# Optimization experiments

Measured on AMD Instinct MI355X. Metric: run time of the kernel, lower is better.

Reference implementation:

```python
import jax, jax.numpy as jnp
import numpy as np

# Standard minigrid color mapping (module references global COLOR_TO_IDX)
COLOR_TO_IDX = {'red': 0, 'green': 1, 'blue': 2, 'purple': 3, 'yellow': 4, 'grey': 5}
AGENT_FEATURE_SIZE = 13
NUM_AGENTS_PER_COLOR = {'grey': 4, 'yellow': 4}
COLOR_ORDER = sorted(NUM_AGENTS_PER_COLOR.keys())  # ['grey', 'yellow']
FEATURE_DIM = 256
B, N = 131072, 16
INPUT_DIM = (1 + sum(NUM_AGENTS_PER_COLOR.values())) * AGENT_FEATURE_SIZE  # 117


def setup_inputs() -> dict:
    key = jax.random.key(0)
    ks = jax.random.split(key, 14)
    inp = {
        'query_position': jax.random.normal(ks[0], (B, 2), jnp.float32),
        'query_direction': jax.random.normal(ks[1], (B, 4), jnp.float32),
        'query_abilities': jax.random.normal(ks[2], (B, 2), jnp.float32),
        'query_carried': jax.random.normal(ks[3], (B, 2), jnp.float32),
        'query_status': jax.random.normal(ks[4], (B, 3), jnp.float32),
        'all_agent_positions': jax.random.normal(ks[5], (B, N, 2), jnp.float32),
        'all_agent_directions': jax.random.normal(ks[6], (B, N, 4), jnp.float32),
        'all_agent_abilities': jax.random.normal(ks[7], (B, N, 2), jnp.float32),
        'all_agent_carried': jax.random.normal(ks[8], (B, N, 2), jnp.float32),
        'all_agent_status': jax.random.normal(ks[9], (B, N, 3), jnp.float32),
        'agent_color_indices': jax.random.randint(ks[10], (B, N), 0, 6, jnp.int32),
        # fc params; W stored (in, out) so y = x @ W + b (same math as torch Linear)
        'W': jax.random.normal(ks[11], (INPUT_DIM, FEATURE_DIM), jnp.float32) / np.sqrt(INPUT_DIM),
        'b': jax.random.normal(ks[12], (FEATURE_DIM,), jnp.float32) * 0.01,
    }
    return inp


def reference(query_position, query_direction, query_abilities, query_carried,
              query_status, all_agent_positions, all_agent_directions,
              all_agent_abilities, all_agent_carried, all_agent_status,
              agent_color_indices, W, b):
    batch = query_position.shape[0]
    # (B, N, 13) per-agent features, (B, 13) query features
    F = jnp.concatenate([all_agent_positions, all_agent_directions,
                         all_agent_abilities, all_agent_carried,
                         all_agent_status], axis=-1)
    query = jnp.concatenate([query_position, query_direction, query_abilities,
                             query_carried, query_status], axis=-1)
    feats = [query]
    rows = jnp.arange(batch)[:, None]  # (B, 1) for batched scatter
    for color in COLOR_ORDER:
        cidx = COLOR_TO_IDX[color]
        M = NUM_AGENTS_PER_COLOR[color]
        mask = agent_color_indices == cidx                 # (B, N)
        rank = jnp.cumsum(mask, axis=1) - 1                # slot of each matching agent
        valid = mask & (rank < M)
        slot = jnp.where(valid, rank, M)                   # dump overflow/non-match into slot M
        out = jnp.zeros((batch, M + 1, AGENT_FEATURE_SIZE), F.dtype)
        out = out.at[rows, slot].set(F)                    # unique (b, slot) per valid agent
        feats.append(out[:, :M].reshape(batch, M * AGENT_FEATURE_SIZE))
    x = jnp.concatenate(feats, axis=1)                     # (B, 117)
    return jax.nn.relu(x @ W + b)
```

## Files before the change

kernel.cpp:

```cpp
#include <hip/hip_runtime.h>


#define TM 128
#define XS_LD 136
#define THREADS 512
#define NCOL 256

typedef short short8 __attribute__((ext_vector_type(8)));
typedef float f32x4 __attribute__((ext_vector_type(4)));

__device__ __forceinline__ short f2bf(float x) {
    unsigned u = __builtin_bit_cast(unsigned, x);
    unsigned r = (u + 0x7fffu + ((u >> 16) & 1u)) >> 16;
    return (short)r;
}
__device__ __forceinline__ unsigned pk2(float a, float b) {
    return (unsigned)(unsigned short)f2bf(a) | ((unsigned)(unsigned short)f2bf(b) << 16);
}

__global__ __launch_bounds__(256)
void swz_w_kernel(const float* __restrict__ W, short* __restrict__ Wb) {
    const int idx  = blockIdx.x * 256 + threadIdx.x;
    const int j    = idx & 7;
    const int lane = (idx >> 3) & 63;
    const int ct   = (idx >> 9) & 3;
    const int kt   = (idx >> 11) & 3;
    const int cg   = (idx >> 13) & 3;
    const int kk   = kt * 32 + (lane >> 4) * 8 + j;
    const int u    = kk / 14;
    const int f    = kk - u * 14;
    const int col  = cg * 64 + ct * 16 + (lane & 15);
    float v = 0.f;
    if (u < 9 && f < 13) v = W[(u * 13 + f) * NCOL + col];
    Wb[idx] = f2bf(v);
}

template<bool WS>
__global__ __launch_bounds__(THREADS, 4)
void mga_encoder_kernel(const float* __restrict__ qpos, const float* __restrict__ qdir,
                        const float* __restrict__ qabil, const float* __restrict__ qcarr,
                        const float* __restrict__ qstat,
                        const float* __restrict__ apos, const float* __restrict__ adir,
                        const float* __restrict__ aabil, const float* __restrict__ acarr,
                        const float* __restrict__ astat,
                        const int* __restrict__ cidx,
                        const float* __restrict__ W, const float* __restrict__ bvec,
                        const short* __restrict__ Wb,
                        float* __restrict__ out) {
    __shared__ __align__(16) short Xs[TM * XS_LD];

    const int tid  = threadIdx.x;
    const int wave = tid >> 6;
    const int lane = tid & 63;
    const int ln   = lane & 15;
    const int q    = lane >> 4;
    const int r0w  = (wave & 1) * 64;
    const int cg   = wave >> 1;
    const int c0   = cg * 64;
    const int rowbase = blockIdx.x * TM;

    #pragma unroll
    for (int i = tid; i < TM * 5; i += THREADS) {
        const int row = i / 5, w = i - row * 5;
        *(unsigned*)&Xs[row * XS_LD + 126 + w * 2] = 0u;
    }

    const int rr  = tid >> 4;
    const int u   = tid & 15;
    const int grp = tid & 48;

    int cs[4];
    #pragma unroll
    for (int p = 0; p < 4; p++)
        cs[p] = cidx[((size_t)(rowbase + p * 32 + rr)) * 16 + u];

    #pragma unroll
    for (int p = 0; p < 4; p++) {
        const int r = p * 32 + rr;
        const size_t b = (size_t)(rowbase + r);
        const int c = cs[p];
        const unsigned long long bg = __ballot(c == 5);
        const unsigned long long by = __ballot(c == 4);
        if (u <= 8) {
            float f0=0.f,f1=0.f,f2=0.f,f3=0.f,f4=0.f,f5=0.f,f6=0.f,
                  f7=0.f,f8=0.f,f9=0.f,f10=0.f,f11=0.f,f12=0.f;
            if (u == 0) {
                const float2 qp = ((const float2*)qpos)[b];
                const float4 qd = ((const float4*)qdir)[b];
                const float2 qa = ((const float2*)qabil)[b];
                const float2 qc = ((const float2*)qcarr)[b];
                f0 = qp.x; f1 = qp.y;
                f2 = qd.x; f3 = qd.y; f4 = qd.z; f5 = qd.w;
                f6 = qa.x; f7 = qa.y;
                f8 = qc.x; f9 = qc.y;
                f10 = qstat[b * 3 + 0]; f11 = qstat[b * 3 + 1]; f12 = qstat[b * 3 + 2];
            } else {
                unsigned mm = (unsigned)(((u <= 4) ? bg : by) >> grp) & 0xFFFFu;
                const int rank = (u - 1) & 3;
                mm = (rank > 0) ? (mm & (mm - 1)) : mm;
                mm = (rank > 1) ? (mm & (mm - 1)) : mm;
                mm = (rank > 2) ? (mm & (mm - 1)) : mm;
                const int j = mm ? (__ffs(mm) - 1) : -1;
                if (j >= 0) {
                    const size_t a = b * 16 + (size_t)j;
                    const float2 pp = ((const float2*)apos)[a];
                    const float4 dd = ((const float4*)adir)[a];
                    const float2 ab = ((const float2*)aabil)[a];
                    const float2 ca = ((const float2*)acarr)[a];
                    f0 = pp.x; f1 = pp.y;
                    f2 = dd.x; f3 = dd.y; f4 = dd.z; f5 = dd.w;
                    f6 = ab.x; f7 = ab.y; f8 = ca.x; f9 = ca.y;
                    f10 = astat[a * 3 + 0]; f11 = astat[a * 3 + 1]; f12 = astat[a * 3 + 2];
                }
            }
            unsigned* xd = (unsigned*)&Xs[r * XS_LD + 14 * u];
            xd[0] = pk2(f0, f1);   xd[1] = pk2(f2, f3);
            xd[2] = pk2(f4, f5);   xd[3] = pk2(f6, f7);
            xd[4] = pk2(f8, f9);   xd[5] = pk2(f10, f11);
            xd[6] = pk2(f12, 0.f);
        }
    }
    __syncthreads();

    const short8* Wf = (const short8*)Wb;
    #pragma unroll 1
    for (int h = 0; h < 2; h++) {
        short8 bfr[4][2];
        if constexpr (WS) {
            #pragma unroll
            for (int kt = 0; kt < 4; kt++)
                #pragma unroll
                for (int cc = 0; cc < 2; cc++)
                    bfr[kt][cc] = Wf[((cg * 4 + kt) * 4 + 2 * h + cc) * 64 + lane];
        } else {
            #pragma unroll
            for (int kt = 0; kt < 4; kt++)
                #pragma unroll
                for (int cc = 0; cc < 2; cc++) {
                    short8 fr;
                    #pragma unroll
                    for (int j = 0; j < 8; j++) {
                        const int kk = kt * 32 + q * 8 + j;
                        const int uu = kk / 14;
                        const int ff = kk - uu * 14;
                        float v = 0.f;
                        if (uu < 9 && ff < 13)
                            v = W[(uu * 13 + ff) * NCOL + c0 + (2 * h + cc) * 16 + ln];
                        fr[j] = f2bf(v);
                    }
                    bfr[kt][cc] = fr;
                }
        }
        f32x4 bv[2];
        #pragma unroll
        for (int cc = 0; cc < 2; cc++)
            bv[cc] = *(const f32x4*)&bvec[c0 + (2 * h + cc) * 16 + q * 4];

        f32x4 acc[4][2];
        #pragma unroll
        for (int rt = 0; rt < 4; rt++)
            #pragma unroll
            for (int cc = 0; cc < 2; cc++) acc[rt][cc] = (f32x4){0.f, 0.f, 0.f, 0.f};

        #pragma unroll
        for (int kt = 0; kt < 4; kt++) {
            short8 av[4];
            #pragma unroll
            for (int rt = 0; rt < 4; rt++)
                av[rt] = *(const short8*)&Xs[(r0w + rt * 16 + ln) * XS_LD + kt * 32 + q * 8];
            #pragma unroll
            for (int rt = 0; rt < 4; rt++)
                #pragma unroll
                for (int cc = 0; cc < 2; cc++)
                    acc[rt][cc] = __builtin_amdgcn_mfma_f32_16x16x32_bf16(
                        bfr[kt][cc], av[rt], acc[rt][cc], 0, 0, 0);
        }

        #pragma unroll
        for (int rt = 0; rt < 4; rt++) {
            const int row = rowbase + r0w + rt * 16 + ln;
            #pragma unroll
            for (int cc = 0; cc < 2; cc++) {
                const int col = c0 + (2 * h + cc) * 16 + q * 4;
                f32x4 v;
                v[0] = fmaxf(acc[rt][cc][0] + bv[cc][0], 0.f);
                v[1] = fmaxf(acc[rt][cc][1] + bv[cc][1], 0.f);
                v[2] = fmaxf(acc[rt][cc][2] + bv[cc][2], 0.f);
                v[3] = fmaxf(acc[rt][cc][3] + bv[cc][3], 0.f);
                *(f32x4*)&out[(size_t)row * NCOL + col] = v;
            }
        }
    }
}

extern "C" void kernel_launch(void* const* d_in, const int* in_sizes, int n_in,
                              void* d_out, int out_size, void* d_ws, size_t ws_size,
                              hipStream_t stream) {
    const float* qpos  = (const float*)d_in[0];
    const float* qdir  = (const float*)d_in[1];
    const float* qabil = (const float*)d_in[2];
    const float* qcarr = (const float*)d_in[3];
    const float* qstat = (const float*)d_in[4];
    const float* apos  = (const float*)d_in[5];
    const float* adir  = (const float*)d_in[6];
    const float* aabil = (const float*)d_in[7];
    const float* acarr = (const float*)d_in[8];
    const float* astat = (const float*)d_in[9];
    const int*   cidx  = (const int*)d_in[10];
    const float* W     = (const float*)d_in[11];
    const float* bvec  = (const float*)d_in[12];
    float* out = (float*)d_out;

    const int B = in_sizes[0] / 2;
    const int nblocks = B / TM;

    const bool ws_ok = (d_ws != nullptr) && (ws_size >= 32768 * sizeof(short));
    if (ws_ok) {
        swz_w_kernel<<<128, 256, 0, stream>>>(W, (short*)d_ws);
        mga_encoder_kernel<true><<<nblocks, THREADS, 0, stream>>>(
            qpos, qdir, qabil, qcarr, qstat, apos, adir, aabil, acarr, astat,
            cidx, W, bvec, (const short*)d_ws, out);
    } else {
        mga_encoder_kernel<false><<<nblocks, THREADS, 0, stream>>>(
            qpos, qdir, qabil, qcarr, qstat, apos, adir, aabil, acarr, astat,
            cidx, W, bvec, nullptr, out);
    }
}
```

Before: 272.3 us.

## Load all agent features densely and gather selected slots via wave shuffles

Every thread now loads its own agent's features with contiguous accesses (lane u reads agent u of its row), packs them to bf16, and uses __shfl to route the selected agent's data to the output slot lane, instead of scattered data-dependent loads by only 8 lanes. Query features are loaded by a separate set of 128 threads. The aim is coalesced, branch-free global reads at the cost of reading every agent (including unselected ones) and extra shuffle instructions. grp now uses lane bits instead of tid bits, which gives the same value.

```diff
diff --git a/kernel.cpp b/kernel.cpp
--- a/kernel.cpp
+++ b/kernel.cpp
@@ -67,7 +67,23 @@
 
     const int rr  = tid >> 4;
     const int u   = tid & 15;
-    const int grp = tid & 48;
+    const int grp = lane & 48;
+
+    if (tid < TM) {
+        const size_t b = (size_t)(rowbase + tid);
+        const float2 qp = ((const float2*)qpos)[b];
+        const float4 qd = ((const float4*)qdir)[b];
+        const float2 qa = ((const float2*)qabil)[b];
+        const float2 qc = ((const float2*)qcarr)[b];
+        const float s0 = qstat[b * 3 + 0];
+        const float s1 = qstat[b * 3 + 1];
+        const float s2 = qstat[b * 3 + 2];
+        unsigned* xd = (unsigned*)&Xs[tid * XS_LD];
+        xd[0] = pk2(qp.x, qp.y); xd[1] = pk2(qd.x, qd.y);
+        xd[2] = pk2(qd.z, qd.w); xd[3] = pk2(qa.x, qa.y);
+        xd[4] = pk2(qc.x, qc.y); xd[5] = pk2(s0, s1);
+        xd[6] = pk2(s2, 0.f);
+    }
 
     int cs[4];
     #pragma unroll
@@ -78,46 +94,50 @@
     for (int p = 0; p < 4; p++) {
         const int r = p * 32 + rr;
         const size_t b = (size_t)(rowbase + r);
+        const size_t a = b * 16 + (size_t)u;
+
+        const float2 pp = ((const float2*)apos)[a];
+        const float4 dd = ((const float4*)adir)[a];
+        const float2 ab = ((const float2*)aabil)[a];
+        const float2 ca = ((const float2*)acarr)[a];
+        const float s0 = astat[a * 3 + 0];
+        const float s1 = astat[a * 3 + 1];
+        const float s2 = astat[a * 3 + 2];
+        unsigned d0 = pk2(pp.x, pp.y), d1 = pk2(dd.x, dd.y);
+        unsigned d2 = pk2(dd.z, dd.w), d3 = pk2(ab.x, ab.y);
+        unsigned d4 = pk2(ca.x, ca.y), d5 = pk2(s0, s1);
+        unsigned d6 = pk2(s2, 0.f);
+
         const int c = cs[p];
         const unsigned long long bg = __ballot(c == 5);
         const unsigned long long by = __ballot(c == 4);
-        if (u <= 8) {
-            float f0=0.f,f1=0.f,f2=0.f,f3=0.f,f4=0.f,f5=0.f,f6=0.f,
-                  f7=0.f,f8=0.f,f9=0.f,f10=0.f,f11=0.f,f12=0.f;
-            if (u == 0) {
-                const float2 qp = ((const float2*)qpos)[b];
-                const float4 qd = ((const float4*)qdir)[b];
-                const float2 qa = ((const float2*)qabil)[b];
-                const float2 qc = ((const float2*)qcarr)[b];
-                f0 = qp.x; f1 = qp.y;
-                f2 = qd.x; f3 = qd.y; f4 = qd.z; f5 = qd.w;
-                f6 = qa.x; f7 = qa.y;
-                f8 = qc.x; f9 = qc.y;
-                f10 = qstat[b * 3 + 0]; f11 = qstat[b * 3 + 1]; f12 = qstat[b * 3 + 2];
-            } else {
-                unsigned mm = (unsigned)(((u <= 4) ? bg : by) >> grp) & 0xFFFFu;
-                const int rank = (u - 1) & 3;
-                mm = (rank > 0) ? (mm & (mm - 1)) : mm;
-                mm = (rank > 1) ? (mm & (mm - 1)) : mm;
-                mm = (rank > 2) ? (mm & (mm - 1)) : mm;
-                const int j = mm ? (__ffs(mm) - 1) : -1;
-                if (j >= 0) {
-                    const size_t a = b * 16 + (size_t)j;
-                    const float2 pp = ((const float2*)apos)[a];
-                    const float4 dd = ((const float4*)adir)[a];
-                    const float2 ab = ((const float2*)aabil)[a];
-                    const float2 ca = ((const float2*)acarr)[a];
-                    f0 = pp.x; f1 = pp.y;
-                    f2 = dd.x; f3 = dd.y; f4 = dd.z; f5 = dd.w;
-                    f6 = ab.x; f7 = ab.y; f8 = ca.x; f9 = ca.y;
-                    f10 = astat[a * 3 + 0]; f11 = astat[a * 3 + 1]; f12 = astat[a * 3 + 2];
-                }
-            }
+
+        int j = -1;
+        if (u >= 1 && u <= 8) {
+            unsigned mm = (unsigned)(((u <= 4) ? bg : by) >> grp) & 0xFFFFu;
+            const int rank = (u - 1) & 3;
+            mm = (rank > 0) ? (mm & (mm - 1)) : mm;
+            mm = (rank > 1) ? (mm & (mm - 1)) : mm;
+            mm = (rank > 2) ? (mm & (mm - 1)) : mm;
+            j = mm ? (__ffs(mm) - 1) : -1;
+        }
+        const int src = grp + (j >= 0 ? j : u);
+
+        unsigned e0 = (unsigned)__shfl((int)d0, src, 64);
+        unsigned e1 = (unsigned)__shfl((int)d1, src, 64);
+        unsigned e2 = (unsigned)__shfl((int)d2, src, 64);
+        unsigned e3 = (unsigned)__shfl((int)d3, src, 64);
+        unsigned e4 = (unsigned)__shfl((int)d4, src, 64);
+        unsigned e5 = (unsigned)__shfl((int)d5, src, 64);
+        unsigned e6 = (unsigned)__shfl((int)d6, src, 64);
+
+        if (u >= 1 && u <= 8) {
+            const bool ok = (j >= 0);
             unsigned* xd = (unsigned*)&Xs[r * XS_LD + 14 * u];
-            xd[0] = pk2(f0, f1);   xd[1] = pk2(f2, f3);
-            xd[2] = pk2(f4, f5);   xd[3] = pk2(f6, f7);
-            xd[4] = pk2(f8, f9);   xd[5] = pk2(f10, f11);
-            xd[6] = pk2(f12, 0.f);
+            xd[0] = ok ? e0 : 0u;  xd[1] = ok ? e1 : 0u;
+            xd[2] = ok ? e2 : 0u;  xd[3] = ok ? e3 : 0u;
+            xd[4] = ok ? e4 : 0u;  xd[5] = ok ? e5 : 0u;
+            xd[6] = ok ? e6 : 0u;
         }
     }
     __syncthreads();
@@ -139,14 +159,14 @@
                 for (int cc = 0; cc < 2; cc++) {
                     short8 fr;
                     #pragma unroll
-                    for (int j = 0; j < 8; j++) {
-                        const int kk = kt * 32 + q * 8 + j;
+                    for (int jj = 0; jj < 8; jj++) {
+                        const int kk = kt * 32 + q * 8 + jj;
                         const int uu = kk / 14;
                         const int ff = kk - uu * 14;
                         float v = 0.f;
                         if (uu < 9 && ff < 13)
                             v = W[(uu * 13 + ff) * NCOL + c0 + (2 * h + cc) * 16 + ln];
-                        fr[j] = f2bf(v);
+                        fr[jj] = f2bf(v);
                     }
                     bfr[kt][cc] = fr;
                 }
```

New measurement: 270.3 us. About the same (-0.8%).
